# Optimization experiments

Measured on AMD Instinct MI355X. Metric: run time of the kernel, lower is better.

## Reference

```python
import jax, jax.numpy as jnp
import numpy as np

SIGMA = 5.0  # matches init_kwargs sigma


def so3_exp_map(w):
    """Rodrigues formula. w: [..., 3] axis-angle -> [..., 3, 3] rotation."""
    theta = jnp.sqrt(jnp.sum(w * w, axis=-1) + 1e-12)            # [...]
    wx, wy, wz = w[..., 0], w[..., 1], w[..., 2]
    z = jnp.zeros_like(wx)
    # normalized skew matrix K = hat(w) / theta
    K = jnp.stack([z, -wz, wy,
                   wz, z, -wx,
                   -wy, wx, z], axis=-1).reshape(w.shape[:-1] + (3, 3))
    K = K / theta[..., None, None]
    s = jnp.sin(theta)[..., None, None]
    c = (1.0 - jnp.cos(theta))[..., None, None]
    I = jnp.eye(3, dtype=w.dtype)
    return I + s * K + c * (K @ K)


def setup_inputs() -> dict:
    key = jax.random.key(0)
    k1, k2, k3, k4, k5 = jax.random.split(key, 5)
    P, N, E = 65536, 512, 4096
    # spread points/control points over a volume where sigma=5 is a meaningful scale
    points = jax.random.normal(k1, (P, 3), dtype=jnp.float32) * 10.0
    control_points = jax.random.normal(k2, (N, 3), dtype=jnp.float32) * 10.0
    rot_vec = jax.random.normal(k3, (N, 3), dtype=jnp.float32) * 0.1
    t = jax.random.normal(k4, (N, 3), dtype=jnp.float32) * 0.1
    edges = jax.random.randint(k5, (E, 2), 0, N, dtype=jnp.int64)
    return {"points": points, "control_points": control_points,
            "rot_vec": rot_vec, "t": t, "edges": edges}


def reference(points, control_points, rot_vec, t, edges):
    # ---- warp_points ----
    # local: [P, N, 3]
    local = points[:, None, :] - control_points[None, :, :]
    skin = jnp.exp(-jnp.sum(local * local, axis=-1) / (2.0 * SIGMA * SIGMA))  # [P, N]
    skin = skin / (jnp.sum(skin, axis=-1, keepdims=True) + 1e-5)
    R = so3_exp_map(rot_vec)                                    # [N, 3, 3]
    warped = (jnp.einsum('nij,pnj->pni', R, local)
              + t[None, :, :] + control_points[None, :, :])     # [P, N, 3]
    warped = jnp.sum(warped * skin[..., None], axis=1)          # [P, 3]
    # ---- reg_term ----
    i, j = edges[:, 0], edges[:, 1]
    ci, cj = control_points[i], control_points[j]               # [E, 3]
    ti, tj = t[i], t[j]
    Ri = R[i]                                                   # [E, 3, 3]
    resid = jnp.einsum('mij,mj->mi', Ri, cj - ci) + ci + ti - (cj + tj)
    reg = jnp.sum(resid * resid)
    return warped, reg
```

## Files before the change

### kernel.cpp

```cpp
#include <hip/hip_runtime.h>
#include <math.h>


constexpr int NP = 65536;
constexpr int PPB = 256;
constexpr float KEXP = -0.02f * 1.44269504088896340736f;
constexpr float M2K  = -2.0f * KEXP;
constexpr float WLOG = 10.0f;
constexpr float EPSS = 1e-5f * 1024.0f;
constexpr float INV2PI = 0.15915494309189535f;

typedef _Float16 half8 __attribute__((ext_vector_type(8)));
typedef float    f32x4 __attribute__((ext_vector_type(4)));

__device__ __forceinline__ float fast_exp2(float x) {
    float r; asm("v_exp_f32 %0, %1" : "=v"(r) : "v"(x)); return r;
}
__device__ __forceinline__ float fast_sin2pi(float x) {
    float r; asm("v_sin_f32 %0, %1" : "=v"(r) : "v"(x)); return r;
}
__device__ __forceinline__ float fast_cos2pi(float x) {
    float r; asm("v_cos_f32 %0, %1" : "=v"(r) : "v"(x)); return r;
}

__device__ __forceinline__ void rodrigues(float wx, float wy, float wz, float* R) {
    float t2 = wx * wx + wy * wy + wz * wz + 1e-12f;
    float th = sqrtf(t2);
    float inv = 1.0f / th;
    float kx = wx * inv, ky = wy * inv, kz = wz * inv;
    float rev = th * INV2PI;
    float s = fast_sin2pi(rev);
    float c = 1.0f - fast_cos2pi(rev);
    float kxky = kx * ky, kxkz = kx * kz, kykz = ky * kz;
    R[0] = 1.0f - c * (ky * ky + kz * kz);
    R[1] = -s * kz + c * kxky;
    R[2] =  s * ky + c * kxkz;
    R[3] =  s * kz + c * kxky;
    R[4] = 1.0f - c * (kx * kx + kz * kz);
    R[5] = -s * kx + c * kykz;
    R[6] = -s * ky + c * kxkz;
    R[7] =  s * kx + c * kykz;
    R[8] = 1.0f - c * (kx * kx + ky * ky);
}

__global__ __launch_bounds__(512) void deform_kernel(
    const float* __restrict__ points,
    const float* __restrict__ cps,
    const float* __restrict__ rot,
    const float* __restrict__ tr,
    const int* __restrict__ edges,
    float* __restrict__ out)
{
    __shared__ float4 ndp[576];
    __shared__ half8 tf[16][64];
    __shared__ float cs[4][2][4][16][17];

    const int tid = threadIdx.x;
    const int bid = blockIdx.x;

    {
        const int n = tid;
        float R[9];
        rodrigues(rot[3 * n], rot[3 * n + 1], rot[3 * n + 2], R);
        float cx = cps[3 * n], cy = cps[3 * n + 1], cz = cps[3 * n + 2];
        float tx = tr[3 * n],  ty = tr[3 * n + 1],  tz = tr[3 * n + 2];
        float bx = tx + cx - (R[0] * cx + R[1] * cy + R[2] * cz);
        float by = ty + cy - (R[3] * cx + R[4] * cy + R[5] * cz);
        float bz = tz + cz - (R[6] * cx + R[7] * cy + R[8] * cz);
        ndp[n + (n >> 3)] = make_float4(M2K * cx, M2K * cy, M2K * cz,
                                        KEXP * (cx * cx + cy * cy + cz * cz) + WLOG);
        float tv[16] = {R[0], R[1], R[2], R[3], R[4], R[5], R[6], R[7], R[8],
                        bx, by, bz, 1.0f, 0.0f, 0.0f, 0.0f};
        const int ks = n >> 5, rr = n & 31, b = rr >> 3, j = rr & 7;
        #pragma unroll
        for (int c = 0; c < 16; ++c) {
            int cc = (c + n) & 15;
            ((_Float16*)&tf[ks][16 * b + cc])[j] = (_Float16)tv[cc];
        }
    }

    if (tid < 16) {
        const int e = bid * 16 + tid;
        const int i  = edges[2 * e + 0];
        const int j2 = edges[2 * e + 1];
        float Ri[9];
        rodrigues(rot[3 * i], rot[3 * i + 1], rot[3 * i + 2], Ri);
        float cix = cps[3 * i], ciy = cps[3 * i + 1], ciz = cps[3 * i + 2];
        float cjx = cps[3 * j2], cjy = cps[3 * j2 + 1], cjz = cps[3 * j2 + 2];
        float dx = cjx - cix, dy = cjy - ciy, dz = cjz - ciz;
        float rx = fmaf(Ri[0], dx, fmaf(Ri[1], dy, Ri[2] * dz)) + cix + tr[3 * i + 0] - cjx - tr[3 * j2 + 0];
        float ry = fmaf(Ri[3], dx, fmaf(Ri[4], dy, Ri[5] * dz)) + ciy + tr[3 * i + 1] - cjy - tr[3 * j2 + 1];
        float rz = fmaf(Ri[6], dx, fmaf(Ri[7], dy, Ri[8] * dz)) + ciz + tr[3 * i + 2] - cjz - tr[3 * j2 + 2];
        float acc = rx * rx + ry * ry + rz * rz;
        #pragma unroll
        for (int off = 8; off > 0; off >>= 1)
            acc += __shfl_down(acc, off, 16);
        if (tid == 0) atomicAdd(out + 3 * NP, acc);
    }

    __syncthreads();

    const int lane = tid & 63;
    const int wv   = tid >> 6;
    const int rg   = wv >> 1;
    const int kh   = wv & 1;
    const int m    = lane & 15;
    const int bq   = lane >> 4;

    const int pbase = bid * PPB + rg * 64 + m;
    float px[4], py[4], pz[4], kp2[4];
    #pragma unroll
    for (int t = 0; t < 4; ++t) {
        int p = pbase + t * 16;
        px[t] = points[3 * p];
        py[t] = points[3 * p + 1];
        pz[t] = points[3 * p + 2];
        kp2[t] = KEXP * (px[t] * px[t] + py[t] * py[t] + pz[t] * pz[t]);
    }

    f32x4 acc[4] = {{0,0,0,0}, {0,0,0,0}, {0,0,0,0}, {0,0,0,0}};

    #pragma unroll 2
    for (int ks = kh * 8; ks < kh * 8 + 8; ++ks) {
        half8 bf = tf[ks][lane];
        const float4* cqp = &ndp[ks * 36 + bq * 9];
        float4 cq[8];
        #pragma unroll
        for (int j = 0; j < 8; ++j) cq[j] = cqp[j];

        #pragma unroll
        for (int t = 0; t < 4; ++t) {
            float w[8];
            #pragma unroll
            for (int j = 0; j < 8; ++j)
                w[j] = fast_exp2(fmaf(cq[j].x, px[t],
                                 fmaf(cq[j].y, py[t],
                                 fmaf(cq[j].z, pz[t], kp2[t] + cq[j].w))));
            union { half8 v; unsigned int u[4]; } a;
            #pragma unroll
            for (int q = 0; q < 4; ++q)
                a.u[q] = __builtin_bit_cast(unsigned int,
                             __builtin_amdgcn_cvt_pkrtz(w[2 * q], w[2 * q + 1]));
            acc[t] = __builtin_amdgcn_mfma_f32_16x16x32_f16(a.v, bf, acc[t], 0, 0, 0);
        }
    }

    #pragma unroll
    for (int t = 0; t < 4; ++t)
        #pragma unroll
        for (int jj = 0; jj < 4; ++jj)
            cs[rg][kh][t][bq * 4 + jj][m] = acc[t][jj];
    __syncthreads();

    if (tid < PPB) {
        const int p = bid * PPB + tid;
        const int rg2 = tid >> 6, w2 = tid & 63, t2 = w2 >> 4, m2 = w2 & 15;
        float c[13];
        #pragma unroll
        for (int i = 0; i < 13; ++i)
            c[i] = cs[rg2][0][t2][m2][i] + cs[rg2][1][t2][m2][i];
        float qx = points[3 * p], qy = points[3 * p + 1], qz = points[3 * p + 2];
        float inv = 1.0f / (c[12] + EPSS);
        float ox = fmaf(c[0], qx, fmaf(c[1], qy, fmaf(c[2], qz, c[9])))  * inv;
        float oy = fmaf(c[3], qx, fmaf(c[4], qy, fmaf(c[5], qz, c[10]))) * inv;
        float oz = fmaf(c[6], qx, fmaf(c[7], qy, fmaf(c[8], qz, c[11]))) * inv;
        out[3 * p + 0] = ox;
        out[3 * p + 1] = oy;
        out[3 * p + 2] = oz;
    }
}

extern "C" void kernel_launch(void* const* d_in, const int* in_sizes, int n_in,
                              void* d_out, int out_size, void* d_ws, size_t ws_size,
                              hipStream_t stream) {
    const float* points = (const float*)d_in[0];
    const float* cps    = (const float*)d_in[1];
    const float* rot    = (const float*)d_in[2];
    const float* tr     = (const float*)d_in[3];
    const int*   edges  = (const int*)d_in[4];
    float* out = (float*)d_out;
    deform_kernel<<<NP / PPB, 512, 0, stream>>>(points, cps, rot, tr, edges, out);
}
```

Measured before the change: 76.29 us.

## Move edge regularizer to epilogue, hoist point loads, raise occupancy hint

Measured after the change: 73.39 us. 3.8% less time.

```diff
diff --git a/kernel.cpp b/kernel.cpp
--- a/kernel.cpp
+++ b/kernel.cpp
@@ -43,7 +43,7 @@
     R[8] = 1.0f - c * (kx * kx + ky * ky);
 }
 
-__global__ __launch_bounds__(512) void deform_kernel(
+__global__ __launch_bounds__(512, 2) void deform_kernel(
     const float* __restrict__ points,
     const float* __restrict__ cps,
     const float* __restrict__ rot,
@@ -57,48 +57,6 @@
 
     const int tid = threadIdx.x;
     const int bid = blockIdx.x;
-
-    {
-        const int n = tid;
-        float R[9];
-        rodrigues(rot[3 * n], rot[3 * n + 1], rot[3 * n + 2], R);
-        float cx = cps[3 * n], cy = cps[3 * n + 1], cz = cps[3 * n + 2];
-        float tx = tr[3 * n],  ty = tr[3 * n + 1],  tz = tr[3 * n + 2];
-        float bx = tx + cx - (R[0] * cx + R[1] * cy + R[2] * cz);
-        float by = ty + cy - (R[3] * cx + R[4] * cy + R[5] * cz);
-        float bz = tz + cz - (R[6] * cx + R[7] * cy + R[8] * cz);
-        ndp[n + (n >> 3)] = make_float4(M2K * cx, M2K * cy, M2K * cz,
-                                        KEXP * (cx * cx + cy * cy + cz * cz) + WLOG);
-        float tv[16] = {R[0], R[1], R[2], R[3], R[4], R[5], R[6], R[7], R[8],
-                        bx, by, bz, 1.0f, 0.0f, 0.0f, 0.0f};
-        const int ks = n >> 5, rr = n & 31, b = rr >> 3, j = rr & 7;
-        #pragma unroll
-        for (int c = 0; c < 16; ++c) {
-            int cc = (c + n) & 15;
-            ((_Float16*)&tf[ks][16 * b + cc])[j] = (_Float16)tv[cc];
-        }
-    }
-
-    if (tid < 16) {
-        const int e = bid * 16 + tid;
-        const int i  = edges[2 * e + 0];
-        const int j2 = edges[2 * e + 1];
-        float Ri[9];
-        rodrigues(rot[3 * i], rot[3 * i + 1], rot[3 * i + 2], Ri);
-        float cix = cps[3 * i], ciy = cps[3 * i + 1], ciz = cps[3 * i + 2];
-        float cjx = cps[3 * j2], cjy = cps[3 * j2 + 1], cjz = cps[3 * j2 + 2];
-        float dx = cjx - cix, dy = cjy - ciy, dz = cjz - ciz;
-        float rx = fmaf(Ri[0], dx, fmaf(Ri[1], dy, Ri[2] * dz)) + cix + tr[3 * i + 0] - cjx - tr[3 * j2 + 0];
-        float ry = fmaf(Ri[3], dx, fmaf(Ri[4], dy, Ri[5] * dz)) + ciy + tr[3 * i + 1] - cjy - tr[3 * j2 + 1];
-        float rz = fmaf(Ri[6], dx, fmaf(Ri[7], dy, Ri[8] * dz)) + ciz + tr[3 * i + 2] - cjz - tr[3 * j2 + 2];
-        float acc = rx * rx + ry * ry + rz * rz;
-        #pragma unroll
-        for (int off = 8; off > 0; off >>= 1)
-            acc += __shfl_down(acc, off, 16);
-        if (tid == 0) atomicAdd(out + 3 * NP, acc);
-    }
-
-    __syncthreads();
 
     const int lane = tid & 63;
     const int wv   = tid >> 6;
@@ -117,6 +75,38 @@
         pz[t] = points[3 * p + 2];
         kp2[t] = KEXP * (px[t] * px[t] + py[t] * py[t] + pz[t] * pz[t]);
     }
+
+    {
+        const int n = tid;
+        float R[9];
+        rodrigues(rot[3 * n], rot[3 * n + 1], rot[3 * n + 2], R);
+        float cx = cps[3 * n], cy = cps[3 * n + 1], cz = cps[3 * n + 2];
+        float tx = tr[3 * n],  ty = tr[3 * n + 1],  tz = tr[3 * n + 2];
+        float bx = tx + cx - (R[0] * cx + R[1] * cy + R[2] * cz);
+        float by = ty + cy - (R[3] * cx + R[4] * cy + R[5] * cz);
+        float bz = tz + cz - (R[6] * cx + R[7] * cy + R[8] * cz);
+        ndp[n + (n >> 3)] = make_float4(M2K * cx, M2K * cy, M2K * cz,
+                                        KEXP * (cx * cx + cy * cy + cz * cz) + WLOG);
+        const int ks = n >> 5, rr = n & 31, b = rr >> 3, j = rr & 7;
+        _Float16* tb = ((_Float16*)&tf[ks][16 * b]) + j;
+        tb[0 * 8]  = (_Float16)R[0];
+        tb[1 * 8]  = (_Float16)R[1];
+        tb[2 * 8]  = (_Float16)R[2];
+        tb[3 * 8]  = (_Float16)R[3];
+        tb[4 * 8]  = (_Float16)R[4];
+        tb[5 * 8]  = (_Float16)R[5];
+        tb[6 * 8]  = (_Float16)R[6];
+        tb[7 * 8]  = (_Float16)R[7];
+        tb[8 * 8]  = (_Float16)R[8];
+        tb[9 * 8]  = (_Float16)bx;
+        tb[10 * 8] = (_Float16)by;
+        tb[11 * 8] = (_Float16)bz;
+        tb[12 * 8] = (_Float16)1.0f;
+        tb[13 * 8] = (_Float16)0.0f;
+        tb[14 * 8] = (_Float16)0.0f;
+        tb[15 * 8] = (_Float16)0.0f;
+    }
+    __syncthreads();
 
     f32x4 acc[4] = {{0,0,0,0}, {0,0,0,0}, {0,0,0,0}, {0,0,0,0}};
 
@@ -167,6 +157,23 @@
         out[3 * p + 0] = ox;
         out[3 * p + 1] = oy;
         out[3 * p + 2] = oz;
+    } else if (tid < PPB + 16) {
+        const int e = bid * 16 + (tid - PPB);
+        const int i  = edges[2 * e + 0];
+        const int j2 = edges[2 * e + 1];
+        float Ri[9];
+        rodrigues(rot[3 * i], rot[3 * i + 1], rot[3 * i + 2], Ri);
+        float cix = cps[3 * i], ciy = cps[3 * i + 1], ciz = cps[3 * i + 2];
+        float cjx = cps[3 * j2], cjy = cps[3 * j2 + 1], cjz = cps[3 * j2 + 2];
+        float dx = cjx - cix, dy = cjy - ciy, dz = cjz - ciz;
+        float rx = fmaf(Ri[0], dx, fmaf(Ri[1], dy, Ri[2] * dz)) + cix + tr[3 * i + 0] - cjx - tr[3 * j2 + 0];
+        float ry = fmaf(Ri[3], dx, fmaf(Ri[4], dy, Ri[5] * dz)) + ciy + tr[3 * i + 1] - cjy - tr[3 * j2 + 1];
+        float rz = fmaf(Ri[6], dx, fmaf(Ri[7], dy, Ri[8] * dz)) + ciz + tr[3 * i + 2] - cjz - tr[3 * j2 + 2];
+        float acc2 = rx * rx + ry * ry + rz * rz;
+        #pragma unroll
+        for (int off = 8; off > 0; off >>= 1)
+            acc2 += __shfl_down(acc2, off, 16);
+        if (tid == PPB) atomicAdd(out + 3 * NP, acc2);
     }
 }
 
```
